# Kernel optimization log

Hardware: AMD Instinct MI355X
Metric: run time of the kernel (lower is better)

The kernel has to match this reference:

```python
import jax, jax.numpy as jnp
import numpy as np

NUM_LEVELS = 16
MIN_RES = 16
MAX_RES = 256
LOG2_T = 19
TABLE_SIZE = 1 << LOG2_T
F = 2
N = 262144
HASH_INIT_SCALE = 0.001

# Static constants (mirror the torch buffers)
_PRIMES = np.array([1, 2654435761, 805459861, 3674653429], dtype=np.uint32)
_GROWTH = np.exp((np.log(MAX_RES) - np.log(MIN_RES)) / (NUM_LEVELS - 1))
_SCALINGS = np.floor(MIN_RES * _GROWTH ** np.arange(NUM_LEVELS)).astype(np.float32)  # [L]
_HASH_OFFSET = (np.arange(NUM_LEVELS) * TABLE_SIZE).astype(np.int32)  # [L]
_CORNERS = np.array([[(i >> d) & 1 for d in range(4)] for i in range(16)], dtype=np.int32)  # [16,4]


def setup_inputs() -> dict:
    key = jax.random.key(0)
    k1, k2 = jax.random.split(key)
    xyzt = jax.random.uniform(k1, (N, 4), dtype=jnp.float32)  # coords in [0,1)
    hash_table = (jax.random.uniform(k2, (TABLE_SIZE * NUM_LEVELS, F), dtype=jnp.float32) * 2.0 - 1.0) * HASH_INIT_SCALE
    return {"xyzt": xyzt, "hash_table": hash_table}


def reference(xyzt, hash_table):
    # xyzt: [N,4], hash_table: [L*T, F]
    primes = jnp.asarray(_PRIMES)                      # uint32
    scalings = jnp.asarray(_SCALINGS)                  # [L]
    hash_offset = jnp.asarray(_HASH_OFFSET)            # [L]
    corners = jnp.asarray(_CORNERS)                    # [16,4] int32

    scaled = xyzt[:, None, :] * scalings[None, :, None]          # [N,L,4]
    sf = jnp.floor(scaled)
    offset = scaled - sf                                          # [N,L,4]
    # Coordinates are non-negative, so float->uint32 cast is exact for floor/ceil.
    sf_i = sf.astype(jnp.uint32)
    sc_i = jnp.ceil(scaled).astype(jnp.uint32)

    # [N,L,16,4]: pick ceil where corner bit is 1, else floor
    corner_coords = jnp.where(corners[None, None] == 1, sc_i[:, :, None, :], sf_i[:, :, None, :])

    # Hash: the torch code does (coord_i64 * prime) XOR-reduced, then % 2^19.
    # Since 2^19 divides 2^32, only the low 32 bits matter -> uint32 wraparound
    # multiply + xor + mask gives identical results to the int64 computation.
    mult = corner_coords * primes                                 # uint32 wrap mod 2^32
    h = mult[..., 0] ^ mult[..., 1] ^ mult[..., 2] ^ mult[..., 3]
    idx = (h & jnp.uint32(TABLE_SIZE - 1)).astype(jnp.int32) + hash_offset[None, :, None]  # [N,L,16]

    corner_features = hash_table[idx]                             # [N,L,16,F]

    # Quadrilinear interpolation weights
    w = jnp.where(corners[None, None] == 1, offset[:, :, None, :], 1.0 - offset[:, :, None, :])
    w = jnp.prod(w, axis=-1)                                      # [N,L,16]

    interpolated = jnp.sum(corner_features * w[..., None], axis=2)  # [N,L,F]
    return interpolated.reshape(xyzt.shape[0], NUM_LEVELS * F)
```

## Files before the change

### kernel.cpp

```cpp
#include <hip/hip_runtime.h>
#include <math.h>

#define NUM_LEVELS 16
#define LOG2_T 19
#define TABLE_SIZE (1u << LOG2_T)

struct Scalings { float s[NUM_LEVELS]; };

__global__ __launch_bounds__(256) void hashenc_kernel(
    const float4* __restrict__ xyzt,
    const float2* __restrict__ table,
    float2* __restrict__ dst,
    Scalings sc,
    int n_pts,
    int blocks_per_level,
    int use_scratch)
{
    unsigned b = blockIdx.x;
    unsigned level = b / (unsigned)blocks_per_level;
    unsigned chunk = b - level * (unsigned)blocks_per_level;

    int n = (int)(chunk * 256u + threadIdx.x);
    if (n >= n_pts || level >= NUM_LEVELS) return;

    float4 p = xyzt[n];
    float s = sc.s[level];

    float sx = p.x * s, sy = p.y * s, sz = p.z * s, st = p.w * s;
    float fx = floorf(sx), fy = floorf(sy), fz = floorf(sz), ft = floorf(st);
    float ox = sx - fx, oy = sy - fy, oz = sz - fz, ot = st - ft;

    const unsigned P1 = 2654435761u, P2 = 805459861u, P3 = 3674653429u;
    unsigned mx[2] = { (unsigned)fx,      (unsigned)ceilf(sx)      };
    unsigned my[2] = { (unsigned)fy * P1, (unsigned)ceilf(sy) * P1 };
    unsigned mz[2] = { (unsigned)fz * P2, (unsigned)ceilf(sz) * P2 };
    unsigned mt[2] = { (unsigned)ft * P3, (unsigned)ceilf(st) * P3 };
    float wx[2] = { 1.0f - ox, ox };
    float wy[2] = { 1.0f - oy, oy };
    float wz[2] = { 1.0f - oz, oz };
    float wt[2] = { 1.0f - ot, ot };

    unsigned base = level << LOG2_T;

    float2 f[16];
    #pragma unroll
    for (int c = 0; c < 16; ++c) {
        unsigned h = mx[c & 1] ^ my[(c >> 1) & 1] ^ mz[(c >> 2) & 1] ^ mt[(c >> 3) & 1];
        unsigned idx = (h & (TABLE_SIZE - 1u)) + base;
        f[c] = table[idx];
    }

    float a0 = 0.0f, a1 = 0.0f;
    #pragma unroll
    for (int c = 0; c < 16; ++c) {
        float w = wx[c & 1] * wy[(c >> 1) & 1] * wz[(c >> 2) & 1] * wt[(c >> 3) & 1];
        a0 = fmaf(f[c].x, w, a0);
        a1 = fmaf(f[c].y, w, a1);
    }

    if (use_scratch)
        dst[(size_t)level * n_pts + n] = make_float2(a0, a1);
    else
        dst[(size_t)n * NUM_LEVELS + level] = make_float2(a0, a1);
}

__global__ __launch_bounds__(256) void transpose_kernel(
    const float2* __restrict__ ws,
    float4* __restrict__ out,
    int n_pts)
{
    int n = blockIdx.x * 256 + (int)threadIdx.x;
    if (n >= n_pts) return;
    float2 v[NUM_LEVELS];
    #pragma unroll
    for (int l = 0; l < NUM_LEVELS; ++l)
        v[l] = ws[(size_t)l * n_pts + n];
    float4* o = out + (size_t)n * 8;
    #pragma unroll
    for (int i = 0; i < 8; ++i)
        o[i] = make_float4(v[2 * i].x, v[2 * i].y, v[2 * i + 1].x, v[2 * i + 1].y);
}

extern "C" void kernel_launch(void* const* d_in, const int* in_sizes, int n_in,
                              void* d_out, int out_size, void* d_ws, size_t ws_size,
                              hipStream_t stream) {
    const float4* xyzt  = (const float4*)d_in[0];
    const float2* table = (const float2*)d_in[1];
    int n_pts = in_sizes[0] / 4;

    Scalings sc;
    double growth = exp((log(256.0) - log(16.0)) / 15.0);
    for (int l = 0; l < NUM_LEVELS; ++l)
        sc.s[l] = (float)floor(16.0 * pow(growth, (double)l));

    int block = 256;
    int bpl = (n_pts + block - 1) / block;
    int grid = NUM_LEVELS * bpl;

    size_t need = (size_t)NUM_LEVELS * n_pts * sizeof(float2);
    int use_scratch = (d_ws != nullptr && ws_size >= need) ? 1 : 0;

    float2* dst = use_scratch ? (float2*)d_ws : (float2*)d_out;
    hashenc_kernel<<<grid, block, 0, stream>>>(xyzt, table, dst, sc, n_pts, bpl, use_scratch);

    if (use_scratch) {
        transpose_kernel<<<bpl, block, 0, stream>>>((const float2*)d_ws, (float4*)d_out, n_pts);
    }
}
```

Baseline: 247.8 us.

## Merge x-adjacent hash corners into float4 loads and widen transpose kernel

Since the x prime is 1, corners that differ only in x hash to adjacent table slots when floor(x) is even and ceil = floor+1, so both are fetched with one 16-byte load. That halves the gather instructions for those points, and the other points keep two separate loads. The interpolation is refactored to factor the x weights out. The transpose kernel now handles two points per thread with float4 loads, at the cost of a divergent branch and extra register pressure.

```diff
diff --git a/kernel.cpp b/kernel.cpp
--- a/kernel.cpp
+++ b/kernel.cpp
@@ -4,6 +4,7 @@
 #define NUM_LEVELS 16
 #define LOG2_T 19
 #define TABLE_SIZE (1u << LOG2_T)
+#define MASK (TABLE_SIZE - 1u)
 
 struct Scalings { float s[NUM_LEVELS]; };
 
@@ -31,37 +32,76 @@
     float ox = sx - fx, oy = sy - fy, oz = sz - fz, ot = st - ft;
 
     const unsigned P1 = 2654435761u, P2 = 805459861u, P3 = 3674653429u;
-    unsigned mx[2] = { (unsigned)fx,      (unsigned)ceilf(sx)      };
-    unsigned my[2] = { (unsigned)fy * P1, (unsigned)ceilf(sy) * P1 };
-    unsigned mz[2] = { (unsigned)fz * P2, (unsigned)ceilf(sz) * P2 };
-    unsigned mt[2] = { (unsigned)ft * P3, (unsigned)ceilf(st) * P3 };
-    float wx[2] = { 1.0f - ox, ox };
-    float wy[2] = { 1.0f - oy, oy };
-    float wz[2] = { 1.0f - oz, oz };
-    float wt[2] = { 1.0f - ot, ot };
+    unsigned xf = (unsigned)fx, xc = (unsigned)ceilf(sx);
+    unsigned my_[2] = { (unsigned)fy * P1, (unsigned)ceilf(sy) * P1 };
+    unsigned mz_[2] = { (unsigned)fz * P2, (unsigned)ceilf(sz) * P2 };
+    unsigned mt_[2] = { (unsigned)ft * P3, (unsigned)ceilf(st) * P3 };
+    float wx0 = 1.0f - ox, wx1 = ox;
+    float wy_[2] = { 1.0f - oy, oy };
+    float wz_[2] = { 1.0f - oz, oz };
+    float wt_[2] = { 1.0f - ot, ot };
+
+    unsigned rest[8]; float wrest[8];
+    #pragma unroll
+    for (int r = 0; r < 8; ++r) {
+        rest[r]  = my_[r & 1] ^ mz_[(r >> 1) & 1] ^ mt_[(r >> 2) & 1];
+        wrest[r] = wy_[r & 1] * wz_[(r >> 1) & 1] * wt_[(r >> 2) & 1];
+    }
 
     unsigned base = level << LOG2_T;
+    float a0 = 0.0f, a1 = 0.0f;
 
-    float2 f[16];
-    #pragma unroll
-    for (int c = 0; c < 16; ++c) {
-        unsigned h = mx[c & 1] ^ my[(c >> 1) & 1] ^ mz[(c >> 2) & 1] ^ mt[(c >> 3) & 1];
-        unsigned idx = (h & (TABLE_SIZE - 1u)) + base;
-        f[c] = table[idx];
-    }
-
-    float a0 = 0.0f, a1 = 0.0f;
-    #pragma unroll
-    for (int c = 0; c < 16; ++c) {
-        float w = wx[c & 1] * wy[(c >> 1) & 1] * wz[(c >> 2) & 1] * wt[(c >> 3) & 1];
-        a0 = fmaf(f[c].x, w, a0);
-        a1 = fmaf(f[c].y, w, a1);
+    bool merge = ((xf & 1u) == 0u) && (xc == xf + 1u);
+    if (merge) {
+        const float4* t4 = (const float4*)table;
+        #pragma unroll
+        for (int r = 0; r < 8; ++r) {
+            unsigned g = ((xf ^ rest[r]) & MASK) + base;
+            float4 v = t4[g >> 1];
+            bool hi = (g & 1u) != 0u;
+            float c0x = hi ? v.z : v.x, c0y = hi ? v.w : v.y;
+            float c1x = hi ? v.x : v.z, c1y = hi ? v.y : v.w;
+            float wl = wrest[r];
+            a0 = fmaf(wl, fmaf(wx0, c0x, wx1 * c1x), a0);
+            a1 = fmaf(wl, fmaf(wx0, c0y, wx1 * c1y), a1);
+        }
+    } else {
+        #pragma unroll
+        for (int r = 0; r < 8; ++r) {
+            unsigned g0 = ((xf ^ rest[r]) & MASK) + base;
+            unsigned g1 = ((xc ^ rest[r]) & MASK) + base;
+            float2 v0 = table[g0];
+            float2 v1 = table[g1];
+            float wl = wrest[r];
+            a0 = fmaf(wl, fmaf(wx0, v0.x, wx1 * v1.x), a0);
+            a1 = fmaf(wl, fmaf(wx0, v0.y, wx1 * v1.y), a1);
+        }
     }
 
     if (use_scratch)
         dst[(size_t)level * n_pts + n] = make_float2(a0, a1);
     else
         dst[(size_t)n * NUM_LEVELS + level] = make_float2(a0, a1);
+}
+
+__global__ __launch_bounds__(256) void transpose2_kernel(
+    const float4* __restrict__ ws4,
+    float4* __restrict__ out,
+    int n2)
+{
+    int t = blockIdx.x * 256 + (int)threadIdx.x;
+    if (t >= n2) return;
+    float4 v[NUM_LEVELS];
+    #pragma unroll
+    for (int l = 0; l < NUM_LEVELS; ++l)
+        v[l] = ws4[(size_t)l * n2 + t];
+    float4* o = out + (size_t)(2 * t) * 8;
+    #pragma unroll
+    for (int i = 0; i < 8; ++i)
+        o[i] = make_float4(v[2 * i].x, v[2 * i].y, v[2 * i + 1].x, v[2 * i + 1].y);
+    #pragma unroll
+    for (int i = 0; i < 8; ++i)
+        o[8 + i] = make_float4(v[2 * i].z, v[2 * i].w, v[2 * i + 1].z, v[2 * i + 1].w);
 }
 
 __global__ __launch_bounds__(256) void transpose_kernel(
@@ -104,6 +144,12 @@
     hashenc_kernel<<<grid, block, 0, stream>>>(xyzt, table, dst, sc, n_pts, bpl, use_scratch);
 
     if (use_scratch) {
-        transpose_kernel<<<bpl, block, 0, stream>>>((const float2*)d_ws, (float4*)d_out, n_pts);
+        if ((n_pts & 1) == 0) {
+            int n2 = n_pts / 2;
+            int g2 = (n2 + block - 1) / block;
+            transpose2_kernel<<<g2, block, 0, stream>>>((const float4*)d_ws, (float4*)d_out, n2);
+        } else {
+            transpose_kernel<<<bpl, block, 0, stream>>>((const float2*)d_ws, (float4*)d_out, n_pts);
+        }
     }
 }
```

Result: faster. 216.9 us (-12.5%).
